# Kernel tuning notes

Hardware: AMD Instinct MI355X
Metric: run time of the kernel (lower is better)

Reference implementation:

```python
import jax, jax.numpy as jnp
import numpy as np

B, S, D = 2, 1024, 768
H, HD = 12, 64
E, K, F = 8, 2, 3072
EPS = 1e-5


def _ln(x, g, b):
    mu = jnp.mean(x, -1, keepdims=True)
    var = jnp.mean(jnp.square(x - mu), -1, keepdims=True)
    return (x - mu) * jax.lax.rsqrt(var + EPS) * g + b


def setup_inputs() -> dict:
    key = jax.random.key(0)
    ks = jax.random.split(key, 12)
    s = lambda k, shape, sc: jax.random.normal(k, shape, jnp.float32) * sc
    return {
        "hidden_states": s(ks[0], (B, S, D), 1.0),
        "ln1_g": jnp.ones((D,), jnp.float32), "ln1_b": jnp.zeros((D,), jnp.float32),
        "w_attn": s(ks[1], (D, 3 * D), 0.02), "b_attn": jnp.zeros((3 * D,), jnp.float32),
        "w_attnproj": s(ks[2], (D, D), 0.02), "b_attnproj": jnp.zeros((D,), jnp.float32),
        "ln2_g": jnp.ones((D,), jnp.float32), "ln2_b": jnp.zeros((D,), jnp.float32),
        "w_router": s(ks[3], (E, D), 0.01),
        "w_fc": s(ks[4], (E, D, F), 0.02 / E), "b_fc": jnp.zeros((E, F), jnp.float32),
        "w_proj": s(ks[5], (E, F, D), 0.02 / E), "b_proj": jnp.zeros((E, D), jnp.float32),
    }


def reference(hidden_states, ln1_g, ln1_b, w_attn, b_attn, w_attnproj, b_attnproj,
              ln2_g, ln2_b, w_router, w_fc, b_fc, w_proj, b_proj):
    # --- attention sub-block (GPT-2 style, causal) ---
    residual = hidden_states
    x = _ln(hidden_states, ln1_g, ln1_b)
    qkv = x @ w_attn + b_attn                         # [B,S,3D]
    q, k, v = jnp.split(qkv, 3, axis=-1)
    def heads(t):
        return t.reshape(B, S, H, HD).transpose(0, 2, 1, 3)  # [B,H,S,HD]
    q, k, v = heads(q), heads(k), heads(v)
    scores = jnp.einsum("bhqd,bhkd->bhqk", q, k) / np.sqrt(HD).astype(np.float32)
    causal = jnp.tril(jnp.ones((S, S), bool))
    scores = jnp.where(causal, scores, jnp.finfo(scores.dtype).min)
    attn = jax.nn.softmax(scores, axis=-1)
    ctx = jnp.einsum("bhqk,bhkd->bhqd", attn, v)
    ctx = ctx.transpose(0, 2, 1, 3).reshape(B, S, D)
    attn_out = ctx @ w_attnproj + b_attnproj
    hs = attn_out + residual

    # --- MoE FFN sub-block ---
    residual = hs
    x2 = _ln(hs, ln2_g, ln2_b)
    logits = x2 @ w_router.T                          # [B,S,E]
    probs = jax.nn.softmax(logits, axis=-1)
    top_w, top_idx = jax.lax.top_k(probs, K)          # [B,S,K]
    top_w = top_w / jnp.sum(top_w, -1, keepdims=True)
    gates = jnp.sum(jax.nn.one_hot(top_idx, E, dtype=x2.dtype) * top_w[..., None], axis=2)  # [B,S,E]
    h = jax.nn.gelu(jnp.einsum("bsd,edf->bsef", x2, w_fc) + b_fc, approximate=False)
    y = jnp.einsum("bsef,efd->bsed", h, w_proj) + b_proj
    moe_out = jnp.einsum("bse,bsed->bsd", gates, y)
    return moe_out + residual
```

## Files before the change

kernel.cpp:

```cpp
#include <hip/hip_runtime.h>
#include <hip/hip_bf16.h>
#include <math.h>

#define NB 2
#define SEQ 1024
#define DM 768
#define NHEAD 12
#define HDIM 64
#define NEXP 8
#define FF 3072
#define NTOK (NB*SEQ)
#define TDIM (3*DM)
#define LNEPS 1e-5f
#define NSLOT (NTOK*2)

typedef __attribute__((ext_vector_type(8))) short v8s;
typedef __attribute__((ext_vector_type(4))) float v4f;

#define GLDS16(src, dst) \
    __builtin_amdgcn_global_load_lds((const __attribute__((address_space(1))) unsigned int*)(src), \
                                     (__attribute__((address_space(3))) unsigned int*)(dst), 16, 0, 0)

#define BARF() do { asm volatile("" ::: "memory"); __builtin_amdgcn_s_barrier(); asm volatile("" ::: "memory"); } while(0)
#define WAITV(n) asm volatile("s_waitcnt vmcnt(" #n ")" ::: "memory")

static __device__ __forceinline__ float bf2f(unsigned short u){
    return __uint_as_float(((unsigned)u) << 16);
}
static __device__ __forceinline__ unsigned short f2bf(float f){
    unsigned u = __float_as_uint(f);
    u += 0x7fffu + ((u >> 16) & 1u);
    return (unsigned short)(u >> 16);
}
static __device__ __forceinline__ float gelu_exact(float x){
    return 0.5f * x * (1.0f + erff(x * 0.70710678118654752440f));
}

__global__ __launch_bounds__(256) void tconv_kernel(const float* __restrict__ in,
                                                    unsigned short* __restrict__ out,
                                                    int R, int C){
    __shared__ float T[32][33];
    size_t base = (size_t)blockIdx.z * R * C;
    int c0 = blockIdx.x * 32, r0 = blockIdx.y * 32;
    int t = threadIdx.x;
    int tr = t >> 3, tc4 = (t & 7) * 4;
    float4 v = *(const float4*)&in[base + (size_t)(r0 + tr) * C + c0 + tc4];
    T[tr][tc4+0] = v.x; T[tr][tc4+1] = v.y; T[tr][tc4+2] = v.z; T[tr][tc4+3] = v.w;
    __syncthreads();
    int oc = t >> 3, or4 = (t & 7) * 4;
    ushort4 o;
    o.x = f2bf(T[or4+0][oc]); o.y = f2bf(T[or4+1][oc]);
    o.z = f2bf(T[or4+2][oc]); o.w = f2bf(T[or4+3][oc]);
    *(ushort4*)&out[base + (size_t)(c0 + oc) * R + r0 + or4] = o;
}

__global__ __launch_bounds__(256) void ln_b(const float* __restrict__ in,
                                            const float* __restrict__ g,
                                            const float* __restrict__ b,
                                            unsigned short* __restrict__ outb){
    int t = blockIdx.x;
    const float* row = in + (size_t)t * DM;
    int tid = threadIdx.x;
    float v0 = row[tid], v1 = row[tid + 256], v2 = row[tid + 512];
    float s  = v0 + v1 + v2;
    float ss = v0*v0 + v1*v1 + v2*v2;
    for (int off = 32; off; off >>= 1){
        s  += __shfl_down(s, off);
        ss += __shfl_down(ss, off);
    }
    __shared__ float ls[4], lss[4];
    int wid = tid >> 6, lane = tid & 63;
    if (lane == 0){ ls[wid] = s; lss[wid] = ss; }
    __syncthreads();
    if (tid == 0){
        float a = ls[0] + ls[1] + ls[2] + ls[3];
        float c = lss[0] + lss[1] + lss[2] + lss[3];
        float mu = a / (float)DM;
        float var = c / (float)DM - mu * mu;
        ls[0] = mu; lss[0] = rsqrtf(var + LNEPS);
    }
    __syncthreads();
    float mu = ls[0], rs = lss[0];
    unsigned short* obrow = outb + (size_t)t * DM;
    obrow[tid]     = f2bf((v0 - mu) * rs * g[tid]       + b[tid]);
    obrow[tid+256] = f2bf((v1 - mu) * rs * g[tid + 256] + b[tid + 256]);
    obrow[tid+512] = f2bf((v2 - mu) * rs * g[tid + 512] + b[tid + 512]);
}

__global__ __launch_bounds__(256) void ln_router(const float* __restrict__ in,
                                                 const float* __restrict__ g,
                                                 const float* __restrict__ b,
                                                 const float* __restrict__ wr,
                                                 unsigned short* __restrict__ outb,
                                                 int* __restrict__ cnt,
                                                 int* __restrict__ expTok,
                                                 int* __restrict__ tokE,
                                                 int* __restrict__ tokPos,
                                                 float* __restrict__ tokGate){
    int t = blockIdx.x;
    const float* row = in + (size_t)t * DM;
    int tid = threadIdx.x;
    float v0 = row[tid], v1 = row[tid + 256], v2 = row[tid + 512];
    float s  = v0 + v1 + v2;
    float ss = v0*v0 + v1*v1 + v2*v2;
    for (int off = 32; off; off >>= 1){
        s  += __shfl_down(s, off);
        ss += __shfl_down(ss, off);
    }
    __shared__ float ls[4], lss[4];
    __shared__ float wsum[4][NEXP];
    int wid = tid >> 6, lane = tid & 63;
    if (lane == 0){ ls[wid] = s; lss[wid] = ss; }
    __syncthreads();
    if (tid == 0){
        float a = ls[0] + ls[1] + ls[2] + ls[3];
        float c = lss[0] + lss[1] + lss[2] + lss[3];
        float mu = a / (float)DM;
        float var = c / (float)DM - mu * mu;
        ls[0] = mu; lss[0] = rsqrtf(var + LNEPS);
    }
    __syncthreads();
    float mu = ls[0], rs = lss[0];
    float o0 = (v0 - mu) * rs * g[tid]       + b[tid];
    float o1 = (v1 - mu) * rs * g[tid + 256] + b[tid + 256];
    float o2 = (v2 - mu) * rs * g[tid + 512] + b[tid + 512];
    unsigned short* obrow = outb + (size_t)t * DM;
    obrow[tid] = f2bf(o0); obrow[tid+256] = f2bf(o1); obrow[tid+512] = f2bf(o2);
    float p[NEXP];
    #pragma unroll
    for (int e = 0; e < NEXP; e++)
        p[e] = o0*wr[e*DM + tid] + o1*wr[e*DM + tid + 256] + o2*wr[e*DM + tid + 512];
    #pragma unroll
    for (int e = 0; e < NEXP; e++)
        for (int off = 32; off; off >>= 1) p[e] += __shfl_down(p[e], off);
    if (lane == 0){
        #pragma unroll
        for (int e = 0; e < NEXP; e++) wsum[wid][e] = p[e];
    }
    __syncthreads();
    if (tid == 0){
        float lg[NEXP];
        #pragma unroll
        for (int e = 0; e < NEXP; e++)
            lg[e] = wsum[0][e] + wsum[1][e] + wsum[2][e] + wsum[3][e];
        int i0 = 0; float m0 = lg[0];
        #pragma unroll
        for (int e = 1; e < NEXP; e++) if (lg[e] > m0){ m0 = lg[e]; i0 = e; }
        int i1 = -1; float m1 = -INFINITY;
        #pragma unroll
        for (int e = 0; e < NEXP; e++) if (e != i0 && lg[e] > m1){ m1 = lg[e]; i1 = e; }
        float mx = fmaxf(m0, m1);
        float e0 = __expf(m0 - mx), e1 = __expf(m1 - mx);
        float inv = 1.0f / (e0 + e1);
        int p0 = atomicAdd(&cnt[i0], 1);
        int p1 = atomicAdd(&cnt[i1], 1);
        expTok[i0*NTOK + p0] = t;
        expTok[i1*NTOK + p1] = t;
        tokE[t*2]   = i0; tokE[t*2+1]   = i1;
        tokPos[t*2] = p0; tokPos[t*2+1] = p1;
        tokGate[t*2]   = e0 * inv;
        tokGate[t*2+1] = e1 * inv;
    }
}

__global__ __launch_bounds__(256) void mm_qkv(const unsigned short* __restrict__ Ab,
                                              const unsigned short* __restrict__ Bb,
                                              const float* __restrict__ bias,
                                              unsigned short* __restrict__ Qb,
                                              unsigned short* __restrict__ Kb,
                                              unsigned short* __restrict__ Vt){
    __shared__ __align__(16) unsigned short As[2][64*32];
    __shared__ __align__(16) unsigned short Bs[2][128*32];
    int bm = blockIdx.y * 64, bn = blockIdx.x * 128;
    int tid = threadIdx.x, wave = tid >> 6, lane = tid & 63;
    int quad = lane >> 4, l15 = lane & 15;
    int wm = wave >> 1, wn = wave & 1;
    int arow = tid >> 2, achunk = (tid & 3) * 8;
    int lrow = lane >> 2, lchunk = (lane & 3) * 8;
    const unsigned short* aS  = Ab + (size_t)(bm + arow) * DM + achunk;
    const unsigned short* bS0 = Bb + (size_t)(bn +      wave*16 + lrow) * DM + lchunk;
    const unsigned short* bS1 = Bb + (size_t)(bn + 64 + wave*16 + lrow) * DM + lchunk;
    v4f acc[2][4];
    #pragma unroll
    for (int i = 0; i < 2; i++)
        #pragma unroll
        for (int j = 0; j < 4; j++) acc[i][j] = (v4f){0.f,0.f,0.f,0.f};

#define QKV_STAGE(buf, kb) do { \
    GLDS16(aS  + (kb), &As[buf][(wave*16)*32]); \
    GLDS16(bS0 + (kb), &Bs[buf][(     wave*16)*32]); \
    GLDS16(bS1 + (kb), &Bs[buf][(64 + wave*16)*32]); \
} while(0)
#define QKV_COMP(buf) do { \
    v8s a[2], bfr[4]; \
    _Pragma("unroll") \
    for (int i = 0; i < 2; i++) a[i] = *(const v8s*)&As[buf][(wm*32 + i*16 + l15)*32 + quad*8]; \
    _Pragma("unroll") \
    for (int i = 0; i < 4; i++) bfr[i] = *(const v8s*)&Bs[buf][(wn*64 + i*16 + l15)*32 + quad*8]; \
    _Pragma("unroll") \
    for (int mi = 0; mi < 2; mi++) \
        _Pragma("unroll") \
        for (int ni = 0; ni < 4; ni++) \
            acc[mi][ni] = __builtin_amdgcn_mfma_f32_16x16x32_bf16(a[mi], bfr[ni], acc[mi][ni], 0, 0, 0); \
} while(0)

    const int NK = DM/32;
    QKV_STAGE(0, 0);
    #pragma unroll 1
    for (int kt = 0; kt < NK; kt += 2){
        QKV_STAGE(1, (kt+1)*32);
        WAITV(3);
        BARF();
        QKV_COMP(0);
        BARF();
        if (kt + 2 < NK){ QKV_STAGE(0, (kt+2)*32); WAITV(3); }
        else            { WAITV(0); }
        BARF();
        QKV_COMP(1);
        BARF();
    }
    int btyp = bn / DM;
    #pragma unroll
    for (int ni = 0; ni < 4; ni++){
        int n = bn + wn*64 + ni*16 + l15;
        float bb = bias[n];
        int hd = n % DM; int h = hd >> 6; int d = hd & 63;
        #pragma unroll
        for (int mi = 0; mi < 2; mi++){
            int m = bm + wm*32 + mi*16 + quad*4;
            int b = m >> 10, sd = m & 1023;
            size_t bhbase = (size_t)(b*NHEAD + h);
            if (btyp == 0){
                #pragma unroll
                for (int r = 0; r < 4; r++)
                    Qb[(bhbase*SEQ + sd + r)*HDIM + d] = f2bf((acc[mi][ni][r] + bb) * 0.125f);
            } else if (btyp == 1){
                #pragma unroll
                for (int r = 0; r < 4; r++)
                    Kb[(bhbase*SEQ + sd + r)*HDIM + d] = f2bf(acc[mi][ni][r] + bb);
            } else {
                ushort4 o;
                o.x = f2bf(acc[mi][ni][0] + bb); o.y = f2bf(acc[mi][ni][1] + bb);
                o.z = f2bf(acc[mi][ni][2] + bb); o.w = f2bf(acc[mi][ni][3] + bb);
                *(ushort4*)&Vt[(bhbase*HDIM + d)*SEQ + sd] = o;
            }
        }
    }
}

__global__ __launch_bounds__(64) void fattn(const unsigned short* __restrict__ Qb,
                                            const unsigned short* __restrict__ Kb,
                                            const unsigned short* __restrict__ Vt,
                                            unsigned short* __restrict__ ctxb){
    int bh = blockIdx.x >> 5;
    int q0 = (31 - (blockIdx.x & 31)) * 32;
    int h = bh % NHEAD, b = bh / NHEAD;
    int lane = threadIdx.x;
    int quad = lane >> 4, l15 = lane & 15;

    __shared__ __align__(16) unsigned short Plds[32*32];

    const unsigned short* qp = Qb + ((size_t)bh*SEQ + q0 + l15) * HDIM + quad*8;
    v8s qa00 = *(const v8s*)qp;
    v8s qa01 = *(const v8s*)(qp + 32);
    v8s qa10 = *(const v8s*)(qp + 16*HDIM);
    v8s qa11 = *(const v8s*)(qp + 16*HDIM + 32);

    v4f o[2][4];
    #pragma unroll
    for (int i = 0; i < 2; i++)
        #pragma unroll
        for (int j = 0; j < 4; j++) o[i][j] = (v4f){0.f,0.f,0.f,0.f};
    float mrow[2][4], lrow[2][4];
    #pragma unroll
    for (int i = 0; i < 2; i++)
        #pragma unroll
        for (int r = 0; r < 4; r++){ mrow[i][r] = -1e30f; lrow[i][r] = 0.f; }

    int nch = (q0 >> 5) + 1;
    for (int ch = 0; ch < nch; ch++){
        int kt = ch * 32;
        const unsigned short* kp = Kb + ((size_t)bh*SEQ + kt + l15) * HDIM + quad*8;
        v8s k00 = *(const v8s*)kp;
        v8s k01 = *(const v8s*)(kp + 32);
        v8s k10 = *(const v8s*)(kp + 16*HDIM);
        v8s k11 = *(const v8s*)(kp + 16*HDIM + 32);
        v4f s00 = {0,0,0,0}, s01 = {0,0,0,0}, s10 = {0,0,0,0}, s11 = {0,0,0,0};
        s00 = __builtin_amdgcn_mfma_f32_16x16x32_bf16(qa00, k00, s00, 0, 0, 0);
        s00 = __builtin_amdgcn_mfma_f32_16x16x32_bf16(qa01, k01, s00, 0, 0, 0);
        s01 = __builtin_amdgcn_mfma_f32_16x16x32_bf16(qa00, k10, s01, 0, 0, 0);
        s01 = __builtin_amdgcn_mfma_f32_16x16x32_bf16(qa01, k11, s01, 0, 0, 0);
        s10 = __builtin_amdgcn_mfma_f32_16x16x32_bf16(qa10, k00, s10, 0, 0, 0);
        s10 = __builtin_amdgcn_mfma_f32_16x16x32_bf16(qa11, k01, s10, 0, 0, 0);
        s11 = __builtin_amdgcn_mfma_f32_16x16x32_bf16(qa10, k10, s11, 0, 0, 0);
        s11 = __builtin_amdgcn_mfma_f32_16x16x32_bf16(qa11, k11, s11, 0, 0, 0);

        int key0 = kt + l15, key1 = kt + 16 + l15;
        float alpha[2][4];
        #pragma unroll
        for (int mi = 0; mi < 2; mi++){
            #pragma unroll
            for (int r = 0; r < 4; r++){
                int qrow = q0 + mi*16 + quad*4 + r;
                float sv0 = mi ? s10[r] : s00[r];
                float sv1 = mi ? s11[r] : s01[r];
                float v0 = (key0 <= qrow) ? sv0 : -1e30f;
                float v1 = (key1 <= qrow) ? sv1 : -1e30f;
                float mx = fmaxf(v0, v1);
                mx = fmaxf(mx, __shfl_xor(mx, 1));
                mx = fmaxf(mx, __shfl_xor(mx, 2));
                mx = fmaxf(mx, __shfl_xor(mx, 4));
                mx = fmaxf(mx, __shfl_xor(mx, 8));
                float mn = fmaxf(mrow[mi][r], mx);
                alpha[mi][r] = __expf(mrow[mi][r] - mn);
                float p0 = __expf(v0 - mn);
                float p1 = __expf(v1 - mn);
                float ps = p0 + p1;
                ps += __shfl_xor(ps, 1);
                ps += __shfl_xor(ps, 2);
                ps += __shfl_xor(ps, 4);
                ps += __shfl_xor(ps, 8);
                lrow[mi][r] = lrow[mi][r] * alpha[mi][r] + ps;
                mrow[mi][r] = mn;
                Plds[(mi*16 + quad*4 + r)*32 + l15]      = f2bf(p0);
                Plds[(mi*16 + quad*4 + r)*32 + 16 + l15] = f2bf(p1);
            }
        }
        #pragma unroll
        for (int mi = 0; mi < 2; mi++)
            #pragma unroll
            for (int df = 0; df < 4; df++)
                #pragma unroll
                for (int r = 0; r < 4; r++)
                    o[mi][df][r] *= alpha[mi][r];
        __syncthreads();
        v8s pa0 = *(const v8s*)&Plds[l15*32 + quad*8];
        v8s pa1 = *(const v8s*)&Plds[(16 + l15)*32 + quad*8];
        const unsigned short* vp = Vt + ((size_t)bh*HDIM + l15) * SEQ + kt + quad*8;
        #pragma unroll
        for (int df = 0; df < 4; df++){
            v8s vb = *(const v8s*)(vp + df*16*SEQ);
            o[0][df] = __builtin_amdgcn_mfma_f32_16x16x32_bf16(pa0, vb, o[0][df], 0, 0, 0);
            o[1][df] = __builtin_amdgcn_mfma_f32_16x16x32_bf16(pa1, vb, o[1][df], 0, 0, 0);
        }
        __syncthreads();
    }
    #pragma unroll
    for (int mi = 0; mi < 2; mi++){
        #pragma unroll
        for (int r = 0; r < 4; r++){
            float inv = 1.0f / lrow[mi][r];
            size_t orow = (size_t)(b*SEQ + q0 + mi*16 + quad*4 + r) * DM + h*HDIM;
            #pragma unroll
            for (int df = 0; df < 4; df++)
                ctxb[orow + df*16 + l15] = f2bf(o[mi][df][r] * inv);
        }
    }
}

__global__ __launch_bounds__(256) void mm_attnproj(const unsigned short* __restrict__ Ab,
                                                   const unsigned short* __restrict__ Bb,
                                                   const float* __restrict__ bias,
                                                   const float* __restrict__ res,
                                                   float* __restrict__ C){
    __shared__ __align__(16) unsigned short As[2][64*32];
    __shared__ __align__(16) unsigned short Bs[2][64*32];
    int bm = blockIdx.y * 64, bn = blockIdx.x * 64;
    int tid = threadIdx.x, wave = tid >> 6, lane = tid & 63;
    int quad = lane >> 4, l15 = lane & 15;
    int wm = wave >> 1, wn = wave & 1;
    int arow = tid >> 2, achunk = (tid & 3) * 8;
    const unsigned short* aS = Ab + (size_t)(bm + arow) * DM + achunk;
    const unsigned short* bS = Bb + (size_t)(bn + arow) * DM + achunk;
    v4f acc[2][2];
    #pragma unroll
    for (int i = 0; i < 2; i++)
        #pragma unroll
        for (int j = 0; j < 2; j++) acc[i][j] = (v4f){0.f,0.f,0.f,0.f};

#define AP_STAGE(buf, kb) do { \
    GLDS16(aS + (kb), &As[buf][(wave*16)*32]); \
    GLDS16(bS + (kb), &Bs[buf][(wave*16)*32]); \
} while(0)
#define AP_COMP(buf) do { \
    v8s a[2], bfr[2]; \
    _Pragma("unroll") \
    for (int i = 0; i < 2; i++){ \
        a[i]   = *(const v8s*)&As[buf][(wm*32 + i*16 + l15)*32 + quad*8]; \
        bfr[i] = *(const v8s*)&Bs[buf][(wn*32 + i*16 + l15)*32 + quad*8]; \
    } \
    _Pragma("unroll") \
    for (int mi = 0; mi < 2; mi++) \
        _Pragma("unroll") \
        for (int ni = 0; ni < 2; ni++) \
            acc[mi][ni] = __builtin_amdgcn_mfma_f32_16x16x32_bf16(a[mi], bfr[ni], acc[mi][ni], 0, 0, 0); \
} while(0)

    const int NK = DM/32;
    AP_STAGE(0, 0);
    #pragma unroll 1
    for (int kt = 0; kt < NK; kt += 2){
        AP_STAGE(1, (kt+1)*32);
        WAITV(2);
        BARF();
        AP_COMP(0);
        BARF();
        if (kt + 2 < NK){ AP_STAGE(0, (kt+2)*32); WAITV(2); }
        else            { WAITV(0); }
        BARF();
        AP_COMP(1);
        BARF();
    }
    #pragma unroll
    for (int ni = 0; ni < 2; ni++){
        int n = bn + wn*32 + ni*16 + l15;
        float bb = bias[n];
        #pragma unroll
        for (int mi = 0; mi < 2; mi++){
            int m = bm + wm*32 + mi*16 + quad*4;
            #pragma unroll
            for (int r = 0; r < 4; r++)
                C[(size_t)(m + r) * DM + n] = acc[mi][ni][r] + bb + res[(size_t)(m + r) * DM + n];
        }
    }
}

__global__ __launch_bounds__(256) void mm_fc(const unsigned short* __restrict__ Xb,
                                             const unsigned short* __restrict__ Wb,
                                             const float* __restrict__ bfc,
                                             const int* __restrict__ expTok,
                                             const int* __restrict__ cnt,
                                             const int* __restrict__ offE,
                                             unsigned short* __restrict__ H){
    int e = blockIdx.z, tile = blockIdx.y;
    int c = cnt[e];
    int rows = c - tile * 128;
    if (rows <= 0) return;
    __shared__ __align__(16) unsigned short As[2][128*32];
    __shared__ __align__(16) unsigned short Bs[2][128*32];
    __shared__ int toks[128];
    int bn = blockIdx.x * 128;
    int tid = threadIdx.x, wave = tid >> 6, lane = tid & 63;
    if (tid < 128){
        int idx = tile * 128 + tid;
        if (idx >= c) idx = c - 1;
        toks[tid] = expTok[e * NTOK + idx];
    }
    __syncthreads();
    int quad = lane >> 4, l15 = lane & 15;
    int wm = wave >> 1, wn = wave & 1;
    int lrow = lane >> 2, lchunk = (lane & 3) * 8;
    int tok0 = toks[     wave*16 + lrow];
    int tok1 = toks[64 + wave*16 + lrow];
    const unsigned short* Be = Wb + (size_t)e * FF * DM;
    const unsigned short* aS0 = Xb + (size_t)tok0 * DM + lchunk;
    const unsigned short* aS1 = Xb + (size_t)tok1 * DM + lchunk;
    const unsigned short* bS0 = Be + (size_t)(bn +      wave*16 + lrow) * DM + lchunk;
    const unsigned short* bS1 = Be + (size_t)(bn + 64 + wave*16 + lrow) * DM + lchunk;
    v4f acc[4][4];
    #pragma unroll
    for (int i = 0; i < 4; i++)
        #pragma unroll
        for (int j = 0; j < 4; j++) acc[i][j] = (v4f){0.f,0.f,0.f,0.f};

#define FC_STAGE(buf, kb) do { \
    GLDS16(aS0 + (kb), &As[buf][(     wave*16)*32]); \
    GLDS16(aS1 + (kb), &As[buf][(64 + wave*16)*32]); \
    GLDS16(bS0 + (kb), &Bs[buf][(     wave*16)*32]); \
    GLDS16(bS1 + (kb), &Bs[buf][(64 + wave*16)*32]); \
} while(0)
#define FC_COMP(buf) do { \
    v8s a[4], bfr[4]; \
    _Pragma("unroll") \
    for (int i = 0; i < 4; i++){ \
        a[i]   = *(const v8s*)&As[buf][(wm*64 + i*16 + l15)*32 + quad*8]; \
        bfr[i] = *(const v8s*)&Bs[buf][(wn*64 + i*16 + l15)*32 + quad*8]; \
    } \
    _Pragma("unroll") \
    for (int mt = 0; mt < 4; mt++) \
        _Pragma("unroll") \
        for (int nt = 0; nt < 4; nt++) \
            acc[mt][nt] = __builtin_amdgcn_mfma_f32_16x16x32_bf16(a[mt], bfr[nt], acc[mt][nt], 0, 0, 0); \
} while(0)

    const int NK = DM/32;
    FC_STAGE(0, 0);
    #pragma unroll 1
    for (int kt = 0; kt < NK; kt += 2){
        FC_STAGE(1, (kt+1)*32);
        WAITV(4);
        BARF();
        FC_COMP(0);
        BARF();
        if (kt + 2 < NK){ FC_STAGE(0, (kt+2)*32); WAITV(4); }
        else            { WAITV(0); }
        BARF();
        FC_COMP(1);
        BARF();
    }
    int slot0 = offE[e] + tile * 128;
    #pragma unroll
    for (int nt = 0; nt < 4; nt++){
        int n = bn + wn*64 + nt*16 + l15;
        float bb = bfc[(size_t)e * FF + n];
        #pragma unroll
        for (int mt = 0; mt < 4; mt++){
            int ml = wm*64 + mt*16 + quad*4;
            #pragma unroll
            for (int r = 0; r < 4; r++)
                if (ml + r < rows)
                    H[(size_t)(slot0 + ml + r) * FF + n] = f2bf(gelu_exact(acc[mt][nt][r] + bb));
        }
    }
}

__global__ __launch_bounds__(256) void mm_proj(const unsigned short* __restrict__ H,
                                               const unsigned short* __restrict__ Wb,
                                               const int* __restrict__ cnt,
                                               const int* __restrict__ offE,
                                               float* __restrict__ Yp){
    int e = blockIdx.z, tile = blockIdx.y;
    int c = cnt[e];
    int rows = c - tile * 64;
    if (rows <= 0) return;
    int sk = blockIdx.x & 1;
    int bn = (blockIdx.x >> 1) * 128;
    __shared__ __align__(16) unsigned short As[2][64*32];
    __shared__ __align__(16) unsigned short Bs[2][128*32];
    int tid = threadIdx.x, wave = tid >> 6, lane = tid & 63;
    int quad = lane >> 4, l15 = lane & 15;
    int wm = wave >> 1, wn = wave & 1;
    int slot0 = offE[e] + tile * 64;
    int arow = tid >> 2, achunk = (tid & 3) * 8;
    int arl = arow < rows ? arow : rows - 1;
    int lrow = lane >> 2, lchunk = (lane & 3) * 8;
    const unsigned short* Be = Wb + (size_t)e * DM * FF;
    const unsigned short* aS  = H  + (size_t)(slot0 + arl) * FF + sk*1536 + achunk;
    const unsigned short* bS0 = Be + (size_t)(bn +      wave*16 + lrow) * FF + sk*1536 + lchunk;
    const unsigned short* bS1 = Be + (size_t)(bn + 64 + wave*16 + lrow) * FF + sk*1536 + lchunk;
    v4f acc[2][4];
    #pragma unroll
    for (int i = 0; i < 2; i++)
        #pragma unroll
        for (int j = 0; j < 4; j++) acc[i][j] = (v4f){0.f,0.f,0.f,0.f};

#define PJ_STAGE(buf, kb) do { \
    GLDS16(aS  + (kb), &As[buf][(wave*16)*32]); \
    GLDS16(bS0 + (kb), &Bs[buf][(     wave*16)*32]); \
    GLDS16(bS1 + (kb), &Bs[buf][(64 + wave*16)*32]); \
} while(0)
#define PJ_COMP(buf) do { \
    v8s a[2], bfr[4]; \
    _Pragma("unroll") \
    for (int i = 0; i < 2; i++) a[i] = *(const v8s*)&As[buf][(wm*32 + i*16 + l15)*32 + quad*8]; \
    _Pragma("unroll") \
    for (int i = 0; i < 4; i++) bfr[i] = *(const v8s*)&Bs[buf][(wn*64 + i*16 + l15)*32 + quad*8]; \
    _Pragma("unroll") \
    for (int mi = 0; mi < 2; mi++) \
        _Pragma("unroll") \
        for (int ni = 0; ni < 4; ni++) \
            acc[mi][ni] = __builtin_amdgcn_mfma_f32_16x16x32_bf16(a[mi], bfr[ni], acc[mi][ni], 0, 0, 0); \
} while(0)

    const int NK = 1536/32;
    PJ_STAGE(0, 0);
    #pragma unroll 1
    for (int kt = 0; kt < NK; kt += 2){
        PJ_STAGE(1, (kt+1)*32);
        WAITV(3);
        BARF();
        PJ_COMP(0);
        BARF();
        if (kt + 2 < NK){ PJ_STAGE(0, (kt+2)*32); WAITV(3); }
        else            { WAITV(0); }
        BARF();
        PJ_COMP(1);
        BARF();
    }
    float* Yo = Yp + (size_t)sk * NSLOT * DM;
    #pragma unroll
    for (int ni = 0; ni < 4; ni++){
        int n = bn + wn*64 + ni*16 + l15;
        #pragma unroll
        for (int mi = 0; mi < 2; mi++){
            int ml = wm*32 + mi*16 + quad*4;
            #pragma unroll
            for (int r = 0; r < 4; r++)
                if (ml + r < rows)
                    Yo[(size_t)(slot0 + ml + r) * DM + n] = acc[mi][ni][r];
        }
    }
}

__global__ void offsets_kernel(const int* __restrict__ cnt, int* __restrict__ offE){
    if (threadIdx.x == 0 && blockIdx.x == 0){
        int a = 0;
        for (int e = 0; e < NEXP; e++){ offE[e] = a; a += cnt[e]; }
    }
}

__global__ __launch_bounds__(256) void combine_kernel(const float* __restrict__ hs,
                                                      const float* __restrict__ Yp,
                                                      const float* __restrict__ bproj,
                                                      const int* __restrict__ tokE,
                                                      const int* __restrict__ tokPos,
                                                      const float* __restrict__ tokGate,
                                                      const int* __restrict__ offE,
                                                      float* __restrict__ out){
    int t = blockIdx.x;
    int e0 = tokE[t*2], e1 = tokE[t*2+1];
    int s0 = offE[e0] + tokPos[t*2];
    int s1 = offE[e1] + tokPos[t*2+1];
    float g0 = tokGate[t*2], g1 = tokGate[t*2+1];
    const float* y0a = Yp + (size_t)s0 * DM;
    const float* y0b = Yp + (size_t)NSLOT * DM + (size_t)s0 * DM;
    const float* y1a = Yp + (size_t)s1 * DM;
    const float* y1b = Yp + (size_t)NSLOT * DM + (size_t)s1 * DM;
    const float* b0 = bproj + (size_t)e0 * DM;
    const float* b1 = bproj + (size_t)e1 * DM;
    const float* hr = hs + (size_t)t * DM;
    float* orow = out + (size_t)t * DM;
    for (int d = threadIdx.x; d < DM; d += 256){
        orow[d] = hr[d] + g0 * (y0a[d] + y0b[d] + b0[d]) + g1 * (y1a[d] + y1b[d] + b1[d]);
    }
}

extern "C" void kernel_launch(void* const* d_in, const int* in_sizes, int n_in,
                              void* d_out, int out_size, void* d_ws, size_t ws_size,
                              hipStream_t stream){
    (void)in_sizes; (void)n_in; (void)out_size; (void)ws_size;
    const float* hidden  = (const float*)d_in[0];
    const float* ln1_g   = (const float*)d_in[1];
    const float* ln1_b   = (const float*)d_in[2];
    const float* w_attn  = (const float*)d_in[3];
    const float* b_attn  = (const float*)d_in[4];
    const float* w_aproj = (const float*)d_in[5];
    const float* b_aproj = (const float*)d_in[6];
    const float* ln2_g   = (const float*)d_in[7];
    const float* ln2_b   = (const float*)d_in[8];
    const float* w_rout  = (const float*)d_in[9];
    const float* w_fc    = (const float*)d_in[10];
    const float* b_fc    = (const float*)d_in[11];
    const float* w_proj  = (const float*)d_in[12];
    const float* b_proj  = (const float*)d_in[13];
    float* out = (float*)d_out;

    char* ws = (char*)d_ws;
    float*          hs   = (float*)(ws + 0);
    unsigned short* xb   = (unsigned short*)(ws + 6291456);
    unsigned short* Qb   = (unsigned short*)(ws + 9437184);
    unsigned short* Kb   = (unsigned short*)(ws + 12582912);
    unsigned short* Vt   = (unsigned short*)(ws + 15728640);
    unsigned short* ctxb = (unsigned short*)(ws + 18874368);
    unsigned short* Wab  = (unsigned short*)(ws + 22020096);
    unsigned short* Wapb = (unsigned short*)(ws + 25559040);
    unsigned short* H    = (unsigned short*)(ws + 9437184);
    unsigned short* Wfcb = (unsigned short*)(ws + 34603008);
    unsigned short* Wprb = (unsigned short*)(ws + 72351744);
    float*          Yp   = (float*)(ws + 34603008);
    char* rt = ws + 110100480;
    int* cnt      = (int*)(rt + 0);
    int* offE     = (int*)(rt + 64);
    int* expTok   = (int*)(rt + 128);
    int* tokE     = (int*)(rt + 128 + 65536);
    int* tokPos   = (int*)(rt + 128 + 81920);
    float* tokGate= (float*)(rt + 128 + 98304);

    hipMemsetAsync(cnt, 0, NEXP * sizeof(int), stream);

    tconv_kernel<<<dim3(TDIM/32, DM/32, 1), 256, 0, stream>>>(w_attn, Wab, DM, TDIM);
    tconv_kernel<<<dim3(DM/32, DM/32, 1), 256, 0, stream>>>(w_aproj, Wapb, DM, DM);
    tconv_kernel<<<dim3(FF/32, DM/32, NEXP), 256, 0, stream>>>(w_fc, Wfcb, DM, FF);
    tconv_kernel<<<dim3(DM/32, FF/32, NEXP), 256, 0, stream>>>(w_proj, Wprb, FF, DM);

    ln_b<<<NTOK, 256, 0, stream>>>(hidden, ln1_g, ln1_b, xb);
    mm_qkv<<<dim3(TDIM/128, NTOK/64), 256, 0, stream>>>(xb, Wab, b_attn, Qb, Kb, Vt);
    fattn<<<NB*NHEAD*32, 64, 0, stream>>>(Qb, Kb, Vt, ctxb);
    mm_attnproj<<<dim3(DM/64, NTOK/64), 256, 0, stream>>>(ctxb, Wapb, b_aproj, hidden, hs);
    ln_router<<<NTOK, 256, 0, stream>>>(hs, ln2_g, ln2_b, w_rout, xb,
                                        cnt, expTok, tokE, tokPos, tokGate);
    offsets_kernel<<<1, 64, 0, stream>>>(cnt, offE);
    mm_fc<<<dim3(FF/128, NTOK/128, NEXP), 256, 0, stream>>>(xb, Wfcb, b_fc, expTok, cnt, offE, H);
    mm_proj<<<dim3((DM/128)*2, NTOK/64, NEXP), 256, 0, stream>>>(H, Wprb, cnt, offE, Yp);
    combine_kernel<<<NTOK, 256, 0, stream>>>(hs, Yp, b_proj, tokE, tokPos, tokGate, offE, out);
}
```

Before: 485.3 us.

## Deepen GEMM pipelines to 4-stage prefetch and shrink MoE FC tile to 64 rows

All four GEMM kernels (qkv, attnproj, fc, proj) move from a double-buffered K loop to a 4-buffer ring that keeps three stages of global-to-LDS loads in flight, with waitcnt thresholds set per remaining iteration. The intent is to hide more global-load latency behind MFMA work. The A-tile loads are also remapped to a per-wave row layout. The MoE FC kernel drops from 128-row to 64-row expert tiles, which cuts padding waste for unevenly loaded experts and launches more blocks, at the cost of less reuse of each B tile. The larger LDS footprint per block may lower occupancy.

```diff
diff --git a/kernel.cpp b/kernel.cpp
--- a/kernel.cpp
+++ b/kernel.cpp
@@ -169,15 +169,14 @@
                                               unsigned short* __restrict__ Qb,
                                               unsigned short* __restrict__ Kb,
                                               unsigned short* __restrict__ Vt){
-    __shared__ __align__(16) unsigned short As[2][64*32];
-    __shared__ __align__(16) unsigned short Bs[2][128*32];
+    __shared__ __align__(16) unsigned short As[4][64*32];
+    __shared__ __align__(16) unsigned short Bs[4][128*32];
     int bm = blockIdx.y * 64, bn = blockIdx.x * 128;
     int tid = threadIdx.x, wave = tid >> 6, lane = tid & 63;
     int quad = lane >> 4, l15 = lane & 15;
     int wm = wave >> 1, wn = wave & 1;
-    int arow = tid >> 2, achunk = (tid & 3) * 8;
     int lrow = lane >> 2, lchunk = (lane & 3) * 8;
-    const unsigned short* aS  = Ab + (size_t)(bm + arow) * DM + achunk;
+    const unsigned short* aS  = Ab + (size_t)(bm +      wave*16 + lrow) * DM + lchunk;
     const unsigned short* bS0 = Bb + (size_t)(bn +      wave*16 + lrow) * DM + lchunk;
     const unsigned short* bS1 = Bb + (size_t)(bn + 64 + wave*16 + lrow) * DM + lchunk;
     v4f acc[2][4];
@@ -186,10 +185,10 @@
         #pragma unroll
         for (int j = 0; j < 4; j++) acc[i][j] = (v4f){0.f,0.f,0.f,0.f};
 
-#define QKV_STAGE(buf, kb) do { \
-    GLDS16(aS  + (kb), &As[buf][(wave*16)*32]); \
-    GLDS16(bS0 + (kb), &Bs[buf][(     wave*16)*32]); \
-    GLDS16(bS1 + (kb), &Bs[buf][(64 + wave*16)*32]); \
+#define QKV_STAGE(buf, kt) do { int kb = (kt)*32; \
+    GLDS16(aS  + kb, &As[buf][(wave*16)*32]); \
+    GLDS16(bS0 + kb, &Bs[buf][(     wave*16)*32]); \
+    GLDS16(bS1 + kb, &Bs[buf][(64 + wave*16)*32]); \
 } while(0)
 #define QKV_COMP(buf) do { \
     v8s a[2], bfr[4]; \
@@ -205,18 +204,16 @@
 } while(0)
 
     const int NK = DM/32;
-    QKV_STAGE(0, 0);
+    QKV_STAGE(0, 0); QKV_STAGE(1, 1); QKV_STAGE(2, 2);
     #pragma unroll 1
-    for (int kt = 0; kt < NK; kt += 2){
-        QKV_STAGE(1, (kt+1)*32);
-        WAITV(3);
-        BARF();
-        QKV_COMP(0);
-        BARF();
-        if (kt + 2 < NK){ QKV_STAGE(0, (kt+2)*32); WAITV(3); }
-        else            { WAITV(0); }
-        BARF();
-        QKV_COMP(1);
+    for (int kt = 0; kt < NK; kt++){
+        int rem = NK - kt;
+        if (rem > 3){ QKV_STAGE((kt+3)&3, kt+3); WAITV(9); }
+        else if (rem == 3){ WAITV(6); }
+        else if (rem == 2){ WAITV(3); }
+        else { WAITV(0); }
+        BARF();
+        QKV_COMP(kt&3);
         BARF();
     }
     int btyp = bn / DM;
@@ -363,24 +360,24 @@
                                                    const float* __restrict__ bias,
                                                    const float* __restrict__ res,
                                                    float* __restrict__ C){
-    __shared__ __align__(16) unsigned short As[2][64*32];
-    __shared__ __align__(16) unsigned short Bs[2][64*32];
+    __shared__ __align__(16) unsigned short As[4][64*32];
+    __shared__ __align__(16) unsigned short Bs[4][64*32];
     int bm = blockIdx.y * 64, bn = blockIdx.x * 64;
     int tid = threadIdx.x, wave = tid >> 6, lane = tid & 63;
     int quad = lane >> 4, l15 = lane & 15;
     int wm = wave >> 1, wn = wave & 1;
-    int arow = tid >> 2, achunk = (tid & 3) * 8;
-    const unsigned short* aS = Ab + (size_t)(bm + arow) * DM + achunk;
-    const unsigned short* bS = Bb + (size_t)(bn + arow) * DM + achunk;
+    int lrow = lane >> 2, lchunk = (lane & 3) * 8;
+    const unsigned short* aS = Ab + (size_t)(bm + wave*16 + lrow) * DM + lchunk;
+    const unsigned short* bS = Bb + (size_t)(bn + wave*16 + lrow) * DM + lchunk;
     v4f acc[2][2];
     #pragma unroll
     for (int i = 0; i < 2; i++)
         #pragma unroll
         for (int j = 0; j < 2; j++) acc[i][j] = (v4f){0.f,0.f,0.f,0.f};
 
-#define AP_STAGE(buf, kb) do { \
-    GLDS16(aS + (kb), &As[buf][(wave*16)*32]); \
-    GLDS16(bS + (kb), &Bs[buf][(wave*16)*32]); \
+#define AP_STAGE(buf, kt) do { int kb = (kt)*32; \
+    GLDS16(aS + kb, &As[buf][(wave*16)*32]); \
+    GLDS16(bS + kb, &Bs[buf][(wave*16)*32]); \
 } while(0)
 #define AP_COMP(buf) do { \
     v8s a[2], bfr[2]; \
@@ -397,18 +394,16 @@
 } while(0)
 
     const int NK = DM/32;
-    AP_STAGE(0, 0);
+    AP_STAGE(0, 0); AP_STAGE(1, 1); AP_STAGE(2, 2);
     #pragma unroll 1
-    for (int kt = 0; kt < NK; kt += 2){
-        AP_STAGE(1, (kt+1)*32);
-        WAITV(2);
-        BARF();
-        AP_COMP(0);
-        BARF();
-        if (kt + 2 < NK){ AP_STAGE(0, (kt+2)*32); WAITV(2); }
-        else            { WAITV(0); }
-        BARF();
-        AP_COMP(1);
+    for (int kt = 0; kt < NK; kt++){
+        int rem = NK - kt;
+        if (rem > 3){ AP_STAGE((kt+3)&3, kt+3); WAITV(6); }
+        else if (rem == 3){ WAITV(4); }
+        else if (rem == 2){ WAITV(2); }
+        else { WAITV(0); }
+        BARF();
+        AP_COMP(kt&3);
         BARF();
     }
     #pragma unroll
@@ -434,15 +429,15 @@
                                              unsigned short* __restrict__ H){
     int e = blockIdx.z, tile = blockIdx.y;
     int c = cnt[e];
-    int rows = c - tile * 128;
+    int rows = c - tile * 64;
     if (rows <= 0) return;
-    __shared__ __align__(16) unsigned short As[2][128*32];
-    __shared__ __align__(16) unsigned short Bs[2][128*32];
-    __shared__ int toks[128];
+    __shared__ __align__(16) unsigned short As[4][64*32];
+    __shared__ __align__(16) unsigned short Bs[4][128*32];
+    __shared__ int toks[64];
     int bn = blockIdx.x * 128;
     int tid = threadIdx.x, wave = tid >> 6, lane = tid & 63;
-    if (tid < 128){
-        int idx = tile * 128 + tid;
+    if (tid < 64){
+        int idx = tile * 64 + tid;
         if (idx >= c) idx = c - 1;
         toks[tid] = expTok[e * NTOK + idx];
     }
@@ -450,66 +445,60 @@
     int quad = lane >> 4, l15 = lane & 15;
     int wm = wave >> 1, wn = wave & 1;
     int lrow = lane >> 2, lchunk = (lane & 3) * 8;
-    int tok0 = toks[     wave*16 + lrow];
-    int tok1 = toks[64 + wave*16 + lrow];
+    int tok0 = toks[wave*16 + lrow];
     const unsigned short* Be = Wb + (size_t)e * FF * DM;
-    const unsigned short* aS0 = Xb + (size_t)tok0 * DM + lchunk;
-    const unsigned short* aS1 = Xb + (size_t)tok1 * DM + lchunk;
+    const unsigned short* aS  = Xb + (size_t)tok0 * DM + lchunk;
     const unsigned short* bS0 = Be + (size_t)(bn +      wave*16 + lrow) * DM + lchunk;
     const unsigned short* bS1 = Be + (size_t)(bn + 64 + wave*16 + lrow) * DM + lchunk;
-    v4f acc[4][4];
-    #pragma unroll
-    for (int i = 0; i < 4; i++)
+    v4f acc[2][4];
+    #pragma unroll
+    for (int i = 0; i < 2; i++)
         #pragma unroll
         for (int j = 0; j < 4; j++) acc[i][j] = (v4f){0.f,0.f,0.f,0.f};
 
-#define FC_STAGE(buf, kb) do { \
-    GLDS16(aS0 + (kb), &As[buf][(     wave*16)*32]); \
-    GLDS16(aS1 + (kb), &As[buf][(64 + wave*16)*32]); \
-    GLDS16(bS0 + (kb), &Bs[buf][(     wave*16)*32]); \
-    GLDS16(bS1 + (kb), &Bs[buf][(64 + wave*16)*32]); \
+#define FC_STAGE(buf, kt) do { int kb = (kt)*32; \
+    GLDS16(aS  + kb, &As[buf][(wave*16)*32]); \
+    GLDS16(bS0 + kb, &Bs[buf][(     wave*16)*32]); \
+    GLDS16(bS1 + kb, &Bs[buf][(64 + wave*16)*32]); \
 } while(0)
 #define FC_COMP(buf) do { \
-    v8s a[4], bfr[4]; \
-    _Pragma("unroll") \
-    for (int i = 0; i < 4; i++){ \
-        a[i]   = *(const v8s*)&As[buf][(wm*64 + i*16 + l15)*32 + quad*8]; \
-        bfr[i] = *(const v8s*)&Bs[buf][(wn*64 + i*16 + l15)*32 + quad*8]; \
-    } \
-    _Pragma("unroll") \
-    for (int mt = 0; mt < 4; mt++) \
+    v8s a[2], bfr[4]; \
+    _Pragma("unroll") \
+    for (int i = 0; i < 2; i++) a[i] = *(const v8s*)&As[buf][(wm*32 + i*16 + l15)*32 + quad*8]; \
+    _Pragma("unroll") \
+    for (int i = 0; i < 4; i++) bfr[i] = *(const v8s*)&Bs[buf][(wn*64 + i*16 + l15)*32 + quad*8]; \
+    _Pragma("unroll") \
+    for (int mi = 0; mi < 2; mi++) \
         _Pragma("unroll") \
-        for (int nt = 0; nt < 4; nt++) \
-            acc[mt][nt] = __builtin_amdgcn_mfma_f32_16x16x32_bf16(a[mt], bfr[nt], acc[mt][nt], 0, 0, 0); \
+        for (int ni = 0; ni < 4; ni++) \
+            acc[mi][ni] = __builtin_amdgcn_mfma_f32_16x16x32_bf16(a[mi], bfr[ni], acc[mi][ni], 0, 0, 0); \
 } while(0)
 
     const int NK = DM/32;
-    FC_STAGE(0, 0);
+    FC_STAGE(0, 0); FC_STAGE(1, 1); FC_STAGE(2, 2);
     #pragma unroll 1
-    for (int kt = 0; kt < NK; kt += 2){
-        FC_STAGE(1, (kt+1)*32);
-        WAITV(4);
-        BARF();
-        FC_COMP(0);
-        BARF();
-        if (kt + 2 < NK){ FC_STAGE(0, (kt+2)*32); WAITV(4); }
-        else            { WAITV(0); }
-        BARF();
-        FC_COMP(1);
-        BARF();
-    }
-    int slot0 = offE[e] + tile * 128;
-    #pragma unroll
-    for (int nt = 0; nt < 4; nt++){
-        int n = bn + wn*64 + nt*16 + l15;
+    for (int kt = 0; kt < NK; kt++){
+        int rem = NK - kt;
+        if (rem > 3){ FC_STAGE((kt+3)&3, kt+3); WAITV(9); }
+        else if (rem == 3){ WAITV(6); }
+        else if (rem == 2){ WAITV(3); }
+        else { WAITV(0); }
+        BARF();
+        FC_COMP(kt&3);
+        BARF();
+    }
+    int slot0 = offE[e] + tile * 64;
+    #pragma unroll
+    for (int ni = 0; ni < 4; ni++){
+        int n = bn + wn*64 + ni*16 + l15;
         float bb = bfc[(size_t)e * FF + n];
         #pragma unroll
-        for (int mt = 0; mt < 4; mt++){
-            int ml = wm*64 + mt*16 + quad*4;
+        for (int mi = 0; mi < 2; mi++){
+            int ml = wm*32 + mi*16 + quad*4;
             #pragma unroll
             for (int r = 0; r < 4; r++)
                 if (ml + r < rows)
-                    H[(size_t)(slot0 + ml + r) * FF + n] = f2bf(gelu_exact(acc[mt][nt][r] + bb));
+                    H[(size_t)(slot0 + ml + r) * FF + n] = f2bf(gelu_exact(acc[mi][ni][r] + bb));
         }
     }
 }
@@ -525,17 +514,17 @@
     if (rows <= 0) return;
     int sk = blockIdx.x & 1;
     int bn = (blockIdx.x >> 1) * 128;
-    __shared__ __align__(16) unsigned short As[2][64*32];
-    __shared__ __align__(16) unsigned short Bs[2][128*32];
+    __shared__ __align__(16) unsigned short As[4][64*32];
+    __shared__ __align__(16) unsigned short Bs[4][128*32];
     int tid = threadIdx.x, wave = tid >> 6, lane = tid & 63;
     int quad = lane >> 4, l15 = lane & 15;
     int wm = wave >> 1, wn = wave & 1;
     int slot0 = offE[e] + tile * 64;
-    int arow = tid >> 2, achunk = (tid & 3) * 8;
+    int lrow = lane >> 2, lchunk = (lane & 3) * 8;
+    int arow = wave*16 + lrow;
     int arl = arow < rows ? arow : rows - 1;
-    int lrow = lane >> 2, lchunk = (lane & 3) * 8;
     const unsigned short* Be = Wb + (size_t)e * DM * FF;
-    const unsigned short* aS  = H  + (size_t)(slot0 + arl) * FF + sk*1536 + achunk;
+    const unsigned short* aS  = H  + (size_t)(slot0 + arl) * FF + sk*1536 + lchunk;
     const unsigned short* bS0 = Be + (size_t)(bn +      wave*16 + lrow) * FF + sk*1536 + lchunk;
     const unsigned short* bS1 = Be + (size_t)(bn + 64 + wave*16 + lrow) * FF + sk*1536 + lchunk;
     v4f acc[2][4];
@@ -544,10 +533,10 @@
         #pragma unroll
         for (int j = 0; j < 4; j++) acc[i][j] = (v4f){0.f,0.f,0.f,0.f};
 
-#define PJ_STAGE(buf, kb) do { \
-    GLDS16(aS  + (kb), &As[buf][(wave*16)*32]); \
-    GLDS16(bS0 + (kb), &Bs[buf][(     wave*16)*32]); \
-    GLDS16(bS1 + (kb), &Bs[buf][(64 + wave*16)*32]); \
+#define PJ_STAGE(buf, kt) do { int kb = (kt)*32; \
+    GLDS16(aS  + kb, &As[buf][(wave*16)*32]); \
+    GLDS16(bS0 + kb, &Bs[buf][(     wave*16)*32]); \
+    GLDS16(bS1 + kb, &Bs[buf][(64 + wave*16)*32]); \
 } while(0)
 #define PJ_COMP(buf) do { \
     v8s a[2], bfr[4]; \
@@ -563,18 +552,16 @@
 } while(0)
 
     const int NK = 1536/32;
-    PJ_STAGE(0, 0);
+    PJ_STAGE(0, 0); PJ_STAGE(1, 1); PJ_STAGE(2, 2);
     #pragma unroll 1
-    for (int kt = 0; kt < NK; kt += 2){
-        PJ_STAGE(1, (kt+1)*32);
-        WAITV(3);
-        BARF();
-        PJ_COMP(0);
-        BARF();
-        if (kt + 2 < NK){ PJ_STAGE(0, (kt+2)*32); WAITV(3); }
-        else            { WAITV(0); }
-        BARF();
-        PJ_COMP(1);
+    for (int kt = 0; kt < NK; kt++){
+        int rem = NK - kt;
+        if (rem > 3){ PJ_STAGE((kt+3)&3, kt+3); WAITV(9); }
+        else if (rem == 3){ WAITV(6); }
+        else if (rem == 2){ WAITV(3); }
+        else { WAITV(0); }
+        BARF();
+        PJ_COMP(kt&3);
         BARF();
     }
     float* Yo = Yp + (size_t)sk * NSLOT * DM;
@@ -680,7 +667,7 @@
     ln_router<<<NTOK, 256, 0, stream>>>(hs, ln2_g, ln2_b, w_rout, xb,
                                         cnt, expTok, tokE, tokPos, tokGate);
     offsets_kernel<<<1, 64, 0, stream>>>(cnt, offE);
-    mm_fc<<<dim3(FF/128, NTOK/128, NEXP), 256, 0, stream>>>(xb, Wfcb, b_fc, expTok, cnt, offE, H);
+    mm_fc<<<dim3(FF/128, NTOK/64, NEXP), 256, 0, stream>>>(xb, Wfcb, b_fc, expTok, cnt, offE, H);
     mm_proj<<<dim3((DM/128)*2, NTOK/64, NEXP), 256, 0, stream>>>(H, Wprb, cnt, offE, Yp);
     combine_kernel<<<NTOK, 256, 0, stream>>>(hs, Yp, b_proj, tokE, tokPos, tokGate, offE, out);
 }
```

After: 493.0 us. No clear change (+1.6%).
